# Kernel tuning notes

Hardware: AMD Instinct MI355X
Metric: run time of the kernel (lower is better)

## Reference

```python
import jax, jax.numpy as jnp
import numpy as np

DIM = 768
NUM_HEADS = 12
HEAD_DIM = DIM // NUM_HEADS
SCALE = HEAD_DIM ** -0.5
TPL = 64  # template_feat_len, fixed by the 1:65 slice in softmax_with_policy


def setup_inputs() -> dict:
    key = jax.random.key(0)
    ks = jax.random.split(key, 16)
    B, S, TOK = 64, 256, 1
    N_v = 1 + 2 * TPL + S  # 385
    w = lambda k, shp: (jax.random.normal(k, shp, dtype=jnp.float32) * 0.02)
    return {
        'x': jax.random.normal(ks[0], (B, N_v, DIM), dtype=jnp.float32),
        'template_mask': jax.random.uniform(ks[1], (B, TPL), dtype=jnp.float32),
        'qkv_w': w(ks[2], (3 * DIM, DIM)),
        'qkv_b': jnp.zeros((3 * DIM,), jnp.float32),
        'proj_w': w(ks[3], (DIM, DIM)),
        'proj_b': jnp.zeros((DIM,), jnp.float32),
        'dp1_w': w(ks[4], (384, 2 * DIM)),
        'dp1_b': jnp.zeros((384,), jnp.float32),
        'dp2_w': w(ks[5], (192, 384)),
        'dp2_b': jnp.zeros((192,), jnp.float32),
        'dp3_w': w(ks[6], (2, 192)),
        'dp3_b': jnp.zeros((2,), jnp.float32),
        'search_feat_len': S,
        'token_len': TOK,
    }


def _forward(x, template_mask, qkv_w, qkv_b, proj_w, proj_b,
             dp1_w, dp1_b, dp2_w, dp2_b, dp3_w, dp3_b,
             search_feat_len, token_len):
    B, N_v, C = x.shape
    S, TOK = search_feat_len, token_len
    tfl = (N_v - 1 - S) // 2          # template_feat_len (== 64)
    N_q = N_v - tfl
    eps = 1e-6

    # --- divide prediction (early=True, tgt_type='allavg') ---
    tgt_rep = jnp.mean(x[:, tfl + TOK: 2 * tfl + TOK], axis=1, keepdims=True)  # [B,1,C]
    tgt_rep = jnp.broadcast_to(tgt_rep, (B, S, C))
    h = jnp.concatenate([x[:, -S:], tgt_rep], axis=-1)                          # [B,S,2C]
    h = jax.nn.gelu(h @ dp1_w.T + dp1_b, approximate=False)
    h = jax.nn.gelu(h @ dp2_w.T + dp2_b, approximate=False)
    divide_prediction = jax.nn.log_softmax(h @ dp3_w.T + dp3_b, axis=-1)        # [B,S,2]

    # eval path: argsort descending -> argmax, one-hot decision
    decision = jax.nn.one_hot(jnp.argmax(divide_prediction, axis=-1), 2,
                              dtype=divide_prediction.dtype)                     # [B,S,2]

    # --- policy assembly [B, N_q, 3] ---
    token_policy = jnp.tile(jnp.array([0., 0., 1.], jnp.float32), (B, TOK, 1))
    template_policy = jnp.tile(jnp.array([1., 0., 0.], jnp.float32),
                               (B, N_q - S - TOK, 1))
    search_policy = jnp.concatenate(
        [jnp.zeros((B, S, 1), decision.dtype), decision], axis=-1)
    policy = jnp.concatenate([token_policy, template_policy, search_policy], axis=1)

    # --- qkv ---
    qkv = (x @ qkv_w.T + qkv_b).reshape(B, N_v, 3, NUM_HEADS, HEAD_DIM)
    qkv = qkv.transpose(2, 0, 3, 1, 4)  # [3,B,H,N_v,hd]
    q_o, k, v = qkv[0], qkv[1], qkv[2]
    q = jnp.concatenate([q_o[:, :, :1], q_o[:, :, tfl + TOK:]], axis=2)  # [B,H,N_q,hd]

    attn = jnp.einsum('bhqd,bhkd->bhqk', q, k) * SCALE  # [B,H,N_q,N_v]

    # --- softmax_with_policy ---
    p0, p1, p2 = policy[..., 0], policy[..., 1], policy[..., 2]
    outer = lambda a, b: jnp.einsum('bi,bj->bij', a, b)
    mask = (outer(p0, p0) + outer(p1, p1)
            + outer(p0, p2) + outer(p1, p2) + outer(p2, p2)
            + outer(p2, p0) + outer(p2, p1))                      # [B,N_q,N_q]
    eye = jnp.eye(N_q, dtype=mask.dtype)
    mask = mask + (1.0 - mask) * eye
    # expand key axis: duplicate template cols (1:65) -> width N_q+64 == N_v
    mask = jnp.concatenate([mask[..., :1], mask[..., 1:65], mask[..., 1:]], axis=-1)
    mask = mask[:, None]                                          # [B,1,N_q,N_v]

    max_att = jnp.max(attn, axis=-1, keepdims=True)
    a = jnp.exp(attn - max_att).astype(jnp.float32) * mask.astype(jnp.float32)
    attn = (a + eps / N_q) / (jnp.sum(a, axis=-1, keepdims=True) + eps)
    attn = attn.astype(max_att.dtype)

    out = jnp.einsum('bhqk,bhkd->bhqd', attn, v)                  # [B,H,N_q,hd]
    out = out.transpose(0, 2, 1, 3).reshape(B, N_q, C)
    return out @ proj_w.T + proj_b


def reference(x, template_mask, qkv_w, qkv_b, proj_w, proj_b,
              dp1_w, dp1_b, dp2_w, dp2_b, dp3_w, dp3_b,
              search_feat_len, token_len):
    return _forward(x, template_mask, qkv_w, qkv_b, proj_w, proj_b,
                    dp1_w, dp1_b, dp2_w, dp2_b, dp3_w, dp3_b,
                    search_feat_len, token_len)
```

## Files before the change

kernel.cpp:

```cpp
#include <hip/hip_runtime.h>
#include <cmath>

typedef unsigned short u16;
typedef unsigned int u32;
typedef __attribute__((ext_vector_type(8))) short short8;
typedef __attribute__((ext_vector_type(4))) float f32x4;

#define B_    64
#define NV    385
#define CDIM  768
#define NQ    321
#define SFL   256
#define NH    12
#define HD    64
#define MQ    (B_*NV)
#define MP    (B_*NQ)
#define MD    (B_*SFL)
#define SCALE_ 0.125f
#define EPS_   1e-6f

__device__ __forceinline__ u16 f2b(float f) {
  u32 x = __float_as_uint(f);
  return (u16)((x + 0x7FFFu + ((x >> 16) & 1u)) >> 16);
}
__device__ __forceinline__ float b2f(u16 h) {
  return __uint_as_float((u32)h << 16);
}

__device__ __forceinline__ void gload_lds16(const void* g, void* l) {
  __builtin_amdgcn_global_load_lds(
      (const __attribute__((address_space(1))) u32*)g,
      (__attribute__((address_space(3))) u32*)l,
      16, 0, 0);
}

__global__ void k_convert4(const float4* __restrict__ in, ushort4* __restrict__ out, int n4) {
  int i = blockIdx.x * blockDim.x + threadIdx.x;
  if (i < n4) {
    float4 v = in[i];
    ushort4 o;
    o.x = f2b(v.x); o.y = f2b(v.y); o.z = f2b(v.z); o.w = f2b(v.w);
    out[i] = o;
  }
}

__global__ void k_gather_split(const float* __restrict__ x, ushort4* __restrict__ hi,
                               ushort4* __restrict__ lo, int n4) {
  int idx = blockIdx.x * blockDim.x + threadIdx.x;
  if (idx < n4) {
    int m = idx / 192, c4 = idx - m*192;
    int b = m >> 8, s = m & 255;
    float4 v = *(const float4*)(x + ((size_t)(b*NV + 129 + s))*CDIM + c4*4);
    ushort4 h, l;
    h.x = f2b(v.x); l.x = f2b(v.x - b2f(h.x));
    h.y = f2b(v.y); l.y = f2b(v.y - b2f(h.y));
    h.z = f2b(v.z); l.z = f2b(v.z - b2f(h.z));
    h.w = f2b(v.w); l.w = f2b(v.w - b2f(h.w));
    hi[idx] = h; lo[idx] = l;
  }
}

__global__ void k_split_w(const float* __restrict__ W, int ldw, int rows, int colsDiv4,
                          int outRows, ushort4* __restrict__ hi, ushort4* __restrict__ lo) {
  int idx = blockIdx.x * blockDim.x + threadIdx.x;
  if (idx < outRows * colsDiv4) {
    int r = idx / colsDiv4, c4 = idx - r*colsDiv4;
    ushort4 h = {0,0,0,0}, l = {0,0,0,0};
    if (r < rows) {
      float4 v = *(const float4*)(W + (size_t)r*ldw + c4*4);
      h.x = f2b(v.x); l.x = f2b(v.x - b2f(h.x));
      h.y = f2b(v.y); l.y = f2b(v.y - b2f(h.y));
      h.z = f2b(v.z); l.z = f2b(v.z - b2f(h.z));
      h.w = f2b(v.w); l.w = f2b(v.w - b2f(h.w));
    }
    hi[idx] = h; lo[idx] = l;
  }
}

__global__ void k_tgt(const float* __restrict__ x, float* __restrict__ tgt) {
  int b = blockIdx.x, c = threadIdx.x;
  float s = 0.f;
  for (int j = 0; j < 64; ++j) s += x[((size_t)(b*NV + 65 + j))*CDIM + c];
  tgt[b*CDIM + c] = s * (1.f/64.f);
}

__device__ __forceinline__ float gelu_exact(float x) {
  return 0.5f * x * (1.f + erff(x * 0.70710678118654752f));
}

__global__ __launch_bounds__(256) void k_gemm128(const u16* __restrict__ A, const u16* __restrict__ W,
                                                 const float* __restrict__ bias,
                                                 u16* __restrict__ Qh, u16* __restrict__ Kh, u16* __restrict__ Vh,
                                                 float* __restrict__ Cf,
                                                 int M, int N, int K, int mode) {
  __shared__ __align__(16) u16 sbuf[128*128];
  u16* As = sbuf;
  u16* Ws = sbuf + 8192;
  int tid = threadIdx.x;
  int wave = tid >> 6, lane = tid & 63;
  int quad = lane >> 4, col = lane & 15;
  int m0 = blockIdx.y * 128, n0 = blockIdx.x * 128;

  const u16* pa[4];
  const u16* pb[4];
#pragma unroll
  for (int p = 0; p < 4; ++p) {
    int c = p*256 + tid;
    int row = c >> 3;
    int sg = (c & 7) ^ (row & 7);
    pa[p] = A + (size_t)min(m0 + row, M - 1) * K + sg*8;
    pb[p] = W + (size_t)(n0 + row) * K + sg*8;
  }

  int wm = (wave >> 1) * 64, wn = (wave & 1) * 64;
  f32x4 acc[4][4];
  f32x4 z4 = {0.f, 0.f, 0.f, 0.f};
#pragma unroll
  for (int i = 0; i < 4; ++i)
#pragma unroll
    for (int j = 0; j < 4; ++j) acc[i][j] = z4;

  for (int k0 = 0; k0 < K; k0 += 64) {
#pragma unroll
    for (int p = 0; p < 4; ++p) {
      gload_lds16(pa[p], &As[(p*256 + wave*64) * 8]);
      gload_lds16(pb[p], &Ws[(p*256 + wave*64) * 8]);
      pa[p] += 64; pb[p] += 64;
    }
    __syncthreads();

#pragma unroll
    for (int kk = 0; kk < 2; ++kk) {
      int sr = quad + kk*4;
      short8 af[4], bf[4];
#pragma unroll
      for (int i = 0; i < 4; ++i) {
        int row = wm + i*16 + col;
        af[i] = *(const short8*)&As[row*64 + ((sr ^ (row & 7)) * 8)];
      }
#pragma unroll
      for (int j = 0; j < 4; ++j) {
        int row = wn + j*16 + col;
        bf[j] = *(const short8*)&Ws[row*64 + ((sr ^ (row & 7)) * 8)];
      }
#pragma unroll
      for (int i = 0; i < 4; ++i)
#pragma unroll
        for (int j = 0; j < 4; ++j)
          acc[i][j] = __builtin_amdgcn_mfma_f32_16x16x32_bf16(af[i], bf[j], acc[i][j], 0, 0, 0);
    }
    __syncthreads();
  }

  if (mode == 0) {
#pragma unroll
    for (int j = 0; j < 4; ++j) {
      int cc = wn + j*16 + col;
      float bv = bias ? bias[n0 + cc] : 0.f;
#pragma unroll
      for (int i = 0; i < 4; ++i)
#pragma unroll
        for (int ii = 0; ii < 4; ++ii) {
          int row = wm + i*16 + quad*4 + ii;
          sbuf[row*128 + cc] = f2b(acc[i][j][ii] + bv);
        }
    }
    __syncthreads();
#pragma unroll
    for (int q = 0; q < 8; ++q) {
      int idx = q*256 + tid;
      int row = idx >> 4, c16 = idx & 15;
      int mg = m0 + row;
      if (mg < M) {
        int n = n0 + c16*8;
        int which = n / 768;
        int rem = n - which*768;
        int hh = rem >> 6, d0 = rem & 63;
        int bb = mg / NV, nn = mg - bb*NV;
        u16* dst = (which == 0) ? Qh : (which == 1) ? Kh : Vh;
        *(float4*)(dst + (((size_t)hh*B_ + bb)*NV + nn)*64 + d0) = *(const float4*)&sbuf[row*128 + c16*8];
      }
    }
  } else {
#pragma unroll
    for (int j = 0; j < 4; ++j) {
      int cc = n0 + wn + j*16 + col;
      float bv = bias ? bias[cc] : 0.f;
#pragma unroll
      for (int i = 0; i < 4; ++i) {
        int r = m0 + wm + i*16 + quad*4;
#pragma unroll
        for (int ii = 0; ii < 4; ++ii) {
          if (r + ii < M) Cf[(size_t)(r + ii) * N + cc] = acc[i][j][ii] + bv;
        }
      }
    }
  }
}

__global__ __launch_bounds__(256) void k_gemm128s(const u16* __restrict__ Ah, const u16* __restrict__ Al,
                                                  const u16* __restrict__ Wh, const u16* __restrict__ Wl,
                                                  const float* __restrict__ bias, const float* __restrict__ bias2,
                                                  u16* __restrict__ Chi, u16* __restrict__ Clo,
                                                  float* __restrict__ Cf,
                                                  int M, int N, int K, int Nb, int geluF) {
  __shared__ __align__(16) u16 sb[4*8192];
  u16* sAh = sb;
  u16* sAl = sb + 8192;
  u16* sWh = sb + 16384;
  u16* sWl = sb + 24576;
  int tid = threadIdx.x;
  int wave = tid >> 6, lane = tid & 63;
  int quad = lane >> 4, col = lane & 15;
  int m0 = blockIdx.y * 128, n0 = blockIdx.x * 128;

  const u16 *pah[4], *pal[4], *pbh[4], *pbl[4];
#pragma unroll
  for (int p = 0; p < 4; ++p) {
    int c = p*256 + tid;
    int row = c >> 3;
    int sg = (c & 7) ^ (row & 7);
    size_t ao = (size_t)min(m0 + row, M - 1) * K + sg*8;
    size_t bo = (size_t)(n0 + row) * K + sg*8;
    pah[p] = Ah + ao; pal[p] = Al + ao;
    pbh[p] = Wh + bo; pbl[p] = Wl + bo;
  }

  int wm = (wave >> 1) * 64, wn = (wave & 1) * 64;
  f32x4 acc[4][4];
  f32x4 z4 = {0.f, 0.f, 0.f, 0.f};
#pragma unroll
  for (int i = 0; i < 4; ++i)
#pragma unroll
    for (int j = 0; j < 4; ++j) acc[i][j] = z4;

  for (int k0 = 0; k0 < K; k0 += 64) {
#pragma unroll
    for (int p = 0; p < 4; ++p) {
      int dst = (p*256 + wave*64) * 8;
      gload_lds16(pah[p], &sAh[dst]);
      gload_lds16(pal[p], &sAl[dst]);
      gload_lds16(pbh[p], &sWh[dst]);
      gload_lds16(pbl[p], &sWl[dst]);
      pah[p] += 64; pal[p] += 64; pbh[p] += 64; pbl[p] += 64;
    }
    __syncthreads();

#pragma unroll
    for (int kk = 0; kk < 2; ++kk) {
      int sr = quad + kk*4;
      short8 ah[4], al[4], bh[4], bl[4];
#pragma unroll
      for (int i = 0; i < 4; ++i) {
        int row = wm + i*16 + col;
        int off = row*64 + ((sr ^ (row & 7)) * 8);
        ah[i] = *(const short8*)&sAh[off];
        al[i] = *(const short8*)&sAl[off];
      }
#pragma unroll
      for (int j = 0; j < 4; ++j) {
        int row = wn + j*16 + col;
        int off = row*64 + ((sr ^ (row & 7)) * 8);
        bh[j] = *(const short8*)&sWh[off];
        bl[j] = *(const short8*)&sWl[off];
      }
#pragma unroll
      for (int i = 0; i < 4; ++i)
#pragma unroll
        for (int j = 0; j < 4; ++j) {
          acc[i][j] = __builtin_amdgcn_mfma_f32_16x16x32_bf16(ah[i], bh[j], acc[i][j], 0, 0, 0);
          acc[i][j] = __builtin_amdgcn_mfma_f32_16x16x32_bf16(ah[i], bl[j], acc[i][j], 0, 0, 0);
          acc[i][j] = __builtin_amdgcn_mfma_f32_16x16x32_bf16(al[i], bh[j], acc[i][j], 0, 0, 0);
        }
    }
    __syncthreads();
  }

  if (geluF) {
#pragma unroll
    for (int j = 0; j < 4; ++j) {
      int cc = wn + j*16 + col;
      float bv = bias ? bias[n0 + cc] : 0.f;
#pragma unroll
      for (int i = 0; i < 4; ++i)
#pragma unroll
        for (int ii = 0; ii < 4; ++ii) {
          int row = wm + i*16 + quad*4 + ii;
          int mg = m0 + row;
          float v = acc[i][j][ii] + bv;
          if (bias2) v += bias2[(size_t)(mg >> 8) * N + n0 + cc];
          v = gelu_exact(v);
          u16 hi = f2b(v);
          sb[row*128 + cc] = hi;
          sb[16384 + row*128 + cc] = f2b(v - b2f(hi));
        }
    }
    __syncthreads();
#pragma unroll
    for (int q = 0; q < 8; ++q) {
      int idx = q*256 + tid;
      int row = idx >> 4, c16 = idx & 15;
      int mg = m0 + row;
      if (mg < M) {
        *(float4*)(Chi + (size_t)mg * N + n0 + c16*8) = *(const float4*)&sb[row*128 + c16*8];
        *(float4*)(Clo + (size_t)mg * N + n0 + c16*8) = *(const float4*)&sb[16384 + row*128 + c16*8];
      }
    }
  } else {
#pragma unroll
    for (int j = 0; j < 4; ++j) {
      int ccg = n0 + wn + j*16 + col;
      float bv = (bias && ccg < Nb) ? bias[ccg] : 0.f;
#pragma unroll
      for (int i = 0; i < 4; ++i) {
        int r = m0 + wm + i*16 + quad*4;
#pragma unroll
        for (int ii = 0; ii < 4; ++ii) {
          if (r + ii < M) Cf[(size_t)(r + ii) * N + ccg] = acc[i][j][ii] + bv;
        }
      }
    }
  }
}

__global__ __launch_bounds__(256) void k_gemm_f32(const float* __restrict__ A,
                                                  const float* __restrict__ x,
                                                  const float* __restrict__ W, int ldw,
                                                  const float* __restrict__ bias,
                                                  float* __restrict__ C, int M, int N, int K,
                                                  int gather, int gelu, int bias2d) {
  __shared__ __align__(16) float As[16][132];
  __shared__ __align__(16) float Ws[16][68];
  int tid = threadIdx.x;
  int tx = tid & 15, ty = tid >> 4;
  int n0 = blockIdx.x * 64, m0 = blockIdx.y * 128;
  float acc[8][4] = {};

  for (int k0 = 0; k0 < K; k0 += 16) {
#pragma unroll
    for (int p = 0; p < 2; ++p) {
      int f = p * 256 + tid;
      int row = f >> 2, kc = (f & 3) * 4;
      float4 v;
      if (gather) {
        int m = m0 + row;
        int b = m >> 8, s2 = m & 255;
        v = *(const float4*)(x + ((size_t)(b*NV + 129 + s2))*CDIM + k0 + kc);
      } else {
        int m = min(m0 + row, M - 1);
        v = *(const float4*)(A + (size_t)m * K + k0 + kc);
      }
      As[kc+0][row] = v.x; As[kc+1][row] = v.y; As[kc+2][row] = v.z; As[kc+3][row] = v.w;
    }
    {
      int row = tid >> 2, kc = (tid & 3) * 4;
      float4 wv = *(const float4*)(W + (size_t)(n0 + row) * ldw + k0 + kc);
      Ws[kc+0][row] = wv.x; Ws[kc+1][row] = wv.y; Ws[kc+2][row] = wv.z; Ws[kc+3][row] = wv.w;
    }
    __syncthreads();
#pragma unroll
    for (int k2 = 0; k2 < 16; ++k2) {
      float4 a0 = *(const float4*)&As[k2][ty*8];
      float4 a1 = *(const float4*)&As[k2][ty*8 + 4];
      float4 wv = *(const float4*)&Ws[k2][tx*4];
      float a_[8] = {a0.x, a0.y, a0.z, a0.w, a1.x, a1.y, a1.z, a1.w};
      float w_[4] = {wv.x, wv.y, wv.z, wv.w};
#pragma unroll
      for (int i = 0; i < 8; ++i)
#pragma unroll
        for (int j = 0; j < 4; ++j) acc[i][j] += a_[i] * w_[j];
    }
    __syncthreads();
  }
#pragma unroll
  for (int i = 0; i < 8; ++i) {
    int r = m0 + ty*8 + i;
    if (r < M) {
      float4 o;
      float* op = (float*)&o;
#pragma unroll
      for (int j = 0; j < 4; ++j) {
        int n = n0 + tx*4 + j;
        float bv = bias2d ? bias[(size_t)(r >> 8) * N + n] : bias[n];
        float v = acc[i][j] + bv;
        op[j] = gelu ? gelu_exact(v) : v;
      }
      *(float4*)(C + (size_t)r * N + n0 + tx*4) = o;
    }
  }
}

__global__ void k_decision(const float* __restrict__ h2f, const float* __restrict__ w3,
                           const float* __restrict__ b3, float* __restrict__ sdec) {
  int r = blockIdx.x * blockDim.x + threadIdx.x;
  const float* hp = h2f + (size_t)r * 256;
  float l0 = b3[0], l1 = b3[1];
  for (int k = 0; k < 192; ++k) {
    float h = gelu_exact(hp[k]);
    l0 += h * w3[k]; l1 += h * w3[192 + k];
  }
  sdec[r] = (l1 > l0) ? 1.f : 0.f;
}

__global__ __launch_bounds__(512, 4) void k_attn(const u16* __restrict__ Qh, const u16* __restrict__ Kh,
                                                 const u16* __restrict__ Vh, const float* __restrict__ sdec,
                                                 u16* __restrict__ O) {
  __shared__ __align__(16) u16 vsT[64*424];
  __shared__ __align__(16) u16 pst[8][16][72];
  __shared__ float sd[256];
  __shared__ __align__(16) float sdm[416];
  __shared__ float vsum[64];
  float* vpart = (float*)pst;

  int b = blockIdx.x, h = blockIdx.y;
  int tid = threadIdx.x;
  int wave = tid >> 6, lane = tid & 63;
  int quad = lane >> 4, col = lane & 15;

  size_t base = ((size_t)(h*B_ + b))*NV*64;
  const u16* Qb = Qh + base;
  const u16* Kb = Kh + base;
  const u16* Vb = Vh + base;

  if (tid < 256) sd[tid] = sdec[b*SFL + tid];
  for (int k = tid; k < 416; k += 512)
    sdm[k] = (k < 129) ? 1.f : ((k <= 384) ? sdec[b*SFL + k - 129] : 0.f);

  for (int i = tid; i < 64*39; i += 512) {
    int d = i / 39, n = 385 + (i - d*39);
    vsT[d*424 + n] = 0;
  }
  for (int idx = tid; idx < NV*8; idx += 512) {
    int n = idx >> 3, seg = idx & 7;
    short8 v = *(const short8*)(Vb + (size_t)n*64 + seg*8);
    int c = n >> 3;
    int cs = (c < 48) ? ((c & ~7) | ((c + seg) & 7)) : c;
    int b2 = cs*8 + (n & 7);
#pragma unroll
    for (int j = 0; j < 8; ++j)
      vsT[(seg*8 + j)*424 + b2] = ((const u16*)&v)[j];
  }
  __syncthreads();

  {
    int d = tid & 63, part = tid >> 6;
    int n_lo = part*49, n_hi = min(n_lo + 49, 385);
    float s = 0.f;
    for (int n = n_lo; n < n_hi; ++n) {
      int c = n >> 3;
      int cs = (c < 48) ? ((c & ~7) | ((c + (d >> 3)) & 7)) : c;
      s += __uint_as_float((u32)vsT[d*424 + cs*8 + (n & 7)] << 16);
    }
    vpart[part*64 + d] = s;
  }
  __syncthreads();
  if (tid < 64) {
    float s = 0.f;
#pragma unroll
    for (int p = 0; p < 8; ++p) s += vpart[p*64 + tid];
    vsum[tid] = s;
  }
  __syncthreads();

  const f32x4 z4 = {0.f, 0.f, 0.f, 0.f};
  float vsn[4];
#pragma unroll
  for (int nt = 0; nt < 4; ++nt) vsn[nt] = vsum[nt*16 + col];

  for (int t = wave; t < 21; t += 8) {
    int qn_lane = t*16 + col;
    int pos = (qn_lane == 0) ? 0 : (min(qn_lane, 320) + 64);
    const u16* qp = Qb + (size_t)pos*64 + quad*8;
    short8 aq0 = *(const short8*)(qp);
    short8 aq1 = *(const short8*)(qp + 32);

    bool isTpl = (qn_lane >= 1 && qn_lane <= 64);
    bool isSearch = (qn_lane >= 65);
    float sdq = isSearch ? sd[min(qn_lane - 65, 255)] : 1.f;

    float m_ = -1e30f, l_ = 0.f;
    f32x4 oc[4];
#pragma unroll
    for (int nt = 0; nt < 4; ++nt) oc[nt] = z4;

    for (int ch = 0; ch < 6; ++ch) {
      int key0c = ch*64;
      f32x4 acc4[4];
#pragma unroll
      for (int j = 0; j < 4; ++j) acc4[j] = z4;
#pragma unroll
      for (int j = 0; j < 4; ++j) {
        const u16* kp = Kb + (size_t)(key0c + j*16 + col)*64;
        short8 k0 = *(const short8*)(kp + quad*8);
        short8 k1 = *(const short8*)(kp + 32 + quad*8);
        acc4[j] = __builtin_amdgcn_mfma_f32_16x16x32_bf16(k0, aq0, acc4[j], 0, 0, 0);
        acc4[j] = __builtin_amdgcn_mfma_f32_16x16x32_bf16(k1, aq1, acc4[j], 0, 0, 0);
      }
      float cm = acc4[0][0];
#pragma unroll
      for (int j = 0; j < 4; ++j)
#pragma unroll
        for (int r = 0; r < 4; ++r)
          if (j || r) cm = fmaxf(cm, acc4[j][r]);
      cm = fmaxf(cm, __shfl_xor(cm, 16, 64));
      cm = fmaxf(cm, __shfl_xor(cm, 32, 64));
      float mn = fmaxf(m_, cm * SCALE_);
      float rnew = __expf(m_ - mn);
      m_ = mn;
      float rb[4];
#pragma unroll
      for (int r = 0; r < 4; ++r) rb[r] = __shfl(rnew, quad*4 + r, 64);
#pragma unroll
      for (int nt = 0; nt < 4; ++nt) {
        oc[nt][0] *= rb[0]; oc[nt][1] *= rb[1]; oc[nt][2] *= rb[2]; oc[nt][3] *= rb[3];
      }

      float ssum = 0.f;
#pragma unroll
      for (int j = 0; j < 4; ++j) {
        int key0 = key0c + j*16;
        float4 tm = make_float4(1.f, 1.f, 1.f, 1.f);
        if (isTpl) tm = *(const float4*)&sdm[key0 + quad*4];
        float a[4];
        const float* tmp = (const float*)&tm;
#pragma unroll
        for (int r = 0; r < 4; ++r) {
          int key = key0 + quad*4 + r;
          float msk = isTpl ? tmp[r]
                            : ((isSearch && key >= 1 && key <= 128) ? sdq : 1.f);
          a[r] = __expf(fmaf(acc4[j][r], SCALE_, -mn)) * msk;
          ssum += a[r];
        }
        uint2 pk;
        pk.x = (u32)f2b(a[0]) | ((u32)f2b(a[1]) << 16);
        pk.y = (u32)f2b(a[2]) | ((u32)f2b(a[3]) << 16);
        *(uint2*)&pst[wave][col][j*16 + quad*4] = pk;
      }
      ssum += __shfl_xor(ssum, 16, 64);
      ssum += __shfl_xor(ssum, 32, 64);
      l_ = l_ * rnew + ssum;

      asm volatile("" ::: "memory");
#pragma unroll
      for (int st = 0; st < 2; ++st) {
        short8 pa = *(const short8*)&pst[wave][col][st*32 + quad*8];
        int step = ch*2 + st;
#pragma unroll
        for (int nt = 0; nt < 4; ++nt) {
          int d = nt*16 + col;
          int c = step*4 + quad;
          int cs = (c & ~7) | ((c + (d >> 3)) & 7);
          short8 bv = *(const short8*)&vsT[d*424 + cs*8];
          oc[nt] = __builtin_amdgcn_mfma_f32_16x16x32_bf16(pa, bv, oc[nt], 0, 0, 0);
        }
      }
    }

    {
      const u16* kp = Kb + (size_t)384*64;
      short8 k0 = *(const short8*)(kp + quad*8);
      short8 k1 = *(const short8*)(kp + 32 + quad*8);
      f32x4 accE = z4;
      accE = __builtin_amdgcn_mfma_f32_16x16x32_bf16(k0, aq0, accE, 0, 0, 0);
      accE = __builtin_amdgcn_mfma_f32_16x16x32_bf16(k1, aq1, accE, 0, 0, 0);
      float cm = (quad == 0) ? accE[0] : -1e30f;
      cm = fmaxf(cm, __shfl_xor(cm, 16, 64));
      cm = fmaxf(cm, __shfl_xor(cm, 32, 64));
      float mn = fmaxf(m_, cm * SCALE_);
      float rnew = __expf(m_ - mn);
      m_ = mn;
      float rb[4];
#pragma unroll
      for (int r = 0; r < 4; ++r) rb[r] = __shfl(rnew, quad*4 + r, 64);
#pragma unroll
      for (int nt = 0; nt < 4; ++nt) {
        oc[nt][0] *= rb[0]; oc[nt][1] *= rb[1]; oc[nt][2] *= rb[2]; oc[nt][3] *= rb[3];
      }
      float mskE = isTpl ? sdm[384] : 1.f;
      float aE = (quad == 0) ? __expf(fmaf(accE[0], SCALE_, -mn)) * mskE : 0.f;
      float ssum = aE;
      ssum += __shfl_xor(ssum, 16, 64);
      ssum += __shfl_xor(ssum, 32, 64);
      l_ = l_ * rnew + ssum;

      uint2 pk;
      pk.x = (quad == 0) ? (u32)f2b(aE) : 0u;
      pk.y = 0u;
      *(uint2*)&pst[wave][col][quad*4] = pk;
      *(uint2*)&pst[wave][col][16 + quad*4] = make_uint2(0u, 0u);
      asm volatile("" ::: "memory");
      short8 pa = *(const short8*)&pst[wave][col][quad*8];
#pragma unroll
      for (int nt = 0; nt < 4; ++nt) {
        int d = nt*16 + col;
        short8 bv = *(const short8*)&vsT[d*424 + (48 + quad)*8];
        oc[nt] = __builtin_amdgcn_mfma_f32_16x16x32_bf16(pa, bv, oc[nt], 0, 0, 0);
      }
    }

    float lb[4];
#pragma unroll
    for (int r = 0; r < 4; ++r) lb[r] = __shfl(l_, quad*4 + r, 64);
    const float epsn = EPS_ / 321.f;
#pragma unroll
    for (int r = 0; r < 4; ++r) {
      float invv = 1.f / (lb[r] + EPS_);
      int qn = t*16 + quad*4 + r;
      if (qn <= 320) {
#pragma unroll
        for (int nt = 0; nt < 4; ++nt) {
          float val = (oc[nt][r] + epsn * vsn[nt]) * invv;
          O[((size_t)(b*NQ + qn))*CDIM + h*HD + nt*16 + col] = f2b(val);
        }
      }
    }
  }
}

extern "C" void kernel_launch(void* const* d_in, const int* in_sizes, int n_in,
                              void* d_out, int out_size, void* d_ws, size_t ws_size,
                              hipStream_t stream) {
  const float* x      = (const float*)d_in[0];
  const float* qkv_w  = (const float*)d_in[2];
  const float* qkv_b  = (const float*)d_in[3];
  const float* proj_w = (const float*)d_in[4];
  const float* proj_b = (const float*)d_in[5];
  const float* dp1_w  = (const float*)d_in[6];
  const float* dp1_b  = (const float*)d_in[7];
  const float* dp2_w  = (const float*)d_in[8];
  const float* dp2_b  = (const float*)d_in[9];
  const float* dp3_w  = (const float*)d_in[10];
  const float* dp3_b  = (const float*)d_in[11];
  float* out = (float*)d_out;

  char* ws = (char*)d_ws;
  size_t off = 0;
  auto alloc = [&](size_t bytes) -> void* {
    void* p = ws + off;
    off += (bytes + 255) & ~(size_t)255;
    return p;
  };
  u16*  xb      = (u16*)alloc((size_t)MQ * CDIM * 2);
  u16*  qkv_wb  = (u16*)alloc((size_t)2304 * CDIM * 2);
  u16*  proj_wb = (u16*)alloc((size_t)CDIM * CDIM * 2);
  u16*  qh      = (u16*)alloc((size_t)NH * B_ * NV * 64 * 2);
  u16*  kh      = (u16*)alloc((size_t)NH * B_ * NV * 64 * 2);
  u16*  vh      = (u16*)alloc((size_t)NH * B_ * NV * 64 * 2);
  u16*  Obuf    = (u16*)alloc((size_t)MP * CDIM * 2);
  float* tgt    = (float*)alloc((size_t)B_ * CDIM * 4);
  float* tb     = (float*)alloc((size_t)B_ * 384 * 4);
  u16*  xsh     = (u16*)alloc((size_t)MD * CDIM * 2);
  u16*  xsl     = (u16*)alloc((size_t)MD * CDIM * 2);
  u16*  w1h     = (u16*)alloc((size_t)384 * CDIM * 2);
  u16*  w1l     = (u16*)alloc((size_t)384 * CDIM * 2);
  u16*  w2h     = (u16*)alloc((size_t)256 * 384 * 2);
  u16*  w2l     = (u16*)alloc((size_t)256 * 384 * 2);
  u16*  h1h     = (u16*)alloc((size_t)MD * 384 * 2);
  u16*  h1l     = (u16*)alloc((size_t)MD * 384 * 2);
  float* h2f    = (float*)alloc((size_t)MD * 256 * 4);
  float* sdec   = (float*)alloc((size_t)MD * 4);

  {
    int n4 = MQ * CDIM / 4;
    k_convert4<<<dim3((n4 + 255)/256), dim3(256), 0, stream>>>((const float4*)x, (ushort4*)xb, n4);
  }
  {
    int n4 = 2304 * CDIM / 4;
    k_convert4<<<dim3((n4 + 255)/256), dim3(256), 0, stream>>>((const float4*)qkv_w, (ushort4*)qkv_wb, n4);
  }
  {
    int n4 = CDIM * CDIM / 4;
    k_convert4<<<dim3((n4 + 255)/256), dim3(256), 0, stream>>>((const float4*)proj_w, (ushort4*)proj_wb, n4);
  }
  k_tgt<<<dim3(B_), dim3(CDIM), 0, stream>>>(x, tgt);

  {
    int n4 = MD * 192;
    k_gather_split<<<dim3((n4 + 255)/256), dim3(256), 0, stream>>>(x, (ushort4*)xsh, (ushort4*)xsl, n4);
  }
  {
    int n4 = 384 * 192;
    k_split_w<<<dim3((n4 + 255)/256), dim3(256), 0, stream>>>(dp1_w, 1536, 384, 192, 384,
                                                              (ushort4*)w1h, (ushort4*)w1l);
  }
  {
    int n4 = 256 * 96;
    k_split_w<<<dim3((n4 + 255)/256), dim3(256), 0, stream>>>(dp2_w, 384, 192, 96, 256,
                                                              (ushort4*)w2h, (ushort4*)w2l);
  }

  k_gemm128<<<dim3(2304/128, (MQ + 127)/128), dim3(256), 0, stream>>>(xb, qkv_wb, qkv_b, qh, kh, vh,
                                                                      (float*)nullptr, MQ, 2304, CDIM, 0);
  k_gemm_f32<<<dim3(384/64, 1), dim3(256), 0, stream>>>(tgt, nullptr, dp1_w + 768, 1536, dp1_b, tb,
                                                        B_, 384, CDIM, 0, 0, 0);
  k_gemm128s<<<dim3(384/128, MD/128), dim3(256), 0, stream>>>(xsh, xsl, w1h, w1l,
                                                              nullptr, tb, h1h, h1l, nullptr,
                                                              MD, 384, CDIM, 384, 1);
  k_gemm128s<<<dim3(256/128, MD/128), dim3(256), 0, stream>>>(h1h, h1l, w2h, w2l,
                                                              dp2_b, nullptr, nullptr, nullptr, h2f,
                                                              MD, 256, 384, 192, 0);
  k_decision<<<dim3(MD/256), dim3(256), 0, stream>>>(h2f, dp3_w, dp3_b, sdec);

  k_attn<<<dim3(B_, NH), dim3(512), 0, stream>>>(qh, kh, vh, sdec, Obuf);

  k_gemm128<<<dim3(CDIM/128, (MP + 127)/128), dim3(256), 0, stream>>>(Obuf, proj_wb, proj_b,
                                                                      nullptr, nullptr, nullptr, out,
                                                                      MP, CDIM, CDIM, 1);
}
```

Baseline: 707.7 us.

## Fuse prep kernels, XCD-swizzle GEMM tiles, parallelize decision, drop eps term

Merges the x conversion and split-gather into one row-wise kernel and the weight conversions into a single launch. Adds XCD-aware block swizzling to the bf16 GEMM, moves the dp2 GELU into the GEMM epilogue, and replaces the per-thread decision loop with a wave-reduced logit difference. Swaps the tiny tgt GEMM for a simple per-batch kernel. In attention it adds s_setprio around the MFMA sections and removes the V-sum eps correction, which slightly changes numerics (drops the eps/N_q term).

```diff
diff --git a/kernel.cpp b/kernel.cpp
--- a/kernel.cpp
+++ b/kernel.cpp
@@ -34,46 +34,76 @@
       16, 0, 0);
 }
 
-__global__ void k_convert4(const float4* __restrict__ in, ushort4* __restrict__ out, int n4) {
-  int i = blockIdx.x * blockDim.x + threadIdx.x;
-  if (i < n4) {
-    float4 v = in[i];
-    ushort4 o;
-    o.x = f2b(v.x); o.y = f2b(v.y); o.z = f2b(v.z); o.w = f2b(v.w);
-    out[i] = o;
-  }
-}
-
-__global__ void k_gather_split(const float* __restrict__ x, ushort4* __restrict__ hi,
-                               ushort4* __restrict__ lo, int n4) {
-  int idx = blockIdx.x * blockDim.x + threadIdx.x;
-  if (idx < n4) {
-    int m = idx / 192, c4 = idx - m*192;
-    int b = m >> 8, s = m & 255;
-    float4 v = *(const float4*)(x + ((size_t)(b*NV + 129 + s))*CDIM + c4*4);
+__device__ __forceinline__ int xcd_swz(int lin, int nwg) {
+  int xcd = lin & 7, idx = lin >> 3;
+  int q = nwg >> 3, r = nwg & 7;
+  int base = (xcd < r) ? xcd * (q + 1) : r * (q + 1) + (xcd - r) * q;
+  return base + idx;
+}
+
+__device__ __forceinline__ float gelu_exact(float x) {
+  return 0.5f * x * (1.f + erff(x * 0.70710678118654752f));
+}
+
+__global__ void k_prep_x(const float* __restrict__ x, ushort4* __restrict__ xb,
+                         ushort4* __restrict__ xsh, ushort4* __restrict__ xsl) {
+  int row = blockIdx.x;
+  int tid = threadIdx.x;
+  float4 v = ((const float4*)x)[(size_t)row*192 + tid];
+  ushort4 h;
+  h.x = f2b(v.x); h.y = f2b(v.y); h.z = f2b(v.z); h.w = f2b(v.w);
+  xb[(size_t)row*192 + tid] = h;
+  int b = row / NV, n = row - b*NV;
+  if (n >= 129) {
+    ushort4 l;
+    l.x = f2b(v.x - b2f(h.x)); l.y = f2b(v.y - b2f(h.y));
+    l.z = f2b(v.z - b2f(h.z)); l.w = f2b(v.w - b2f(h.w));
+    size_t s = (size_t)(b*256 + n - 129)*192 + tid;
+    xsh[s] = h; xsl[s] = l;
+  }
+}
+
+#define PR0 442368
+#define PR1 (PR0 + 147456)
+#define PR2 (PR1 + 73728)
+#define PR3 (PR2 + 24576)
+__global__ void k_prep_w(const float* __restrict__ qkv_w, const float* __restrict__ proj_w,
+                         const float* __restrict__ dp1_w, const float* __restrict__ dp2_w,
+                         ushort4* __restrict__ qkv_wb, ushort4* __restrict__ proj_wb,
+                         ushort4* __restrict__ w1h, ushort4* __restrict__ w1l,
+                         ushort4* __restrict__ w2h, ushort4* __restrict__ w2l) {
+  int i = blockIdx.x * 256 + threadIdx.x;
+  if (i < PR0) {
+    float4 v = ((const float4*)qkv_w)[i];
+    ushort4 h; h.x = f2b(v.x); h.y = f2b(v.y); h.z = f2b(v.z); h.w = f2b(v.w);
+    qkv_wb[i] = h;
+  } else if (i < PR1) {
+    int j = i - PR0;
+    float4 v = ((const float4*)proj_w)[j];
+    ushort4 h; h.x = f2b(v.x); h.y = f2b(v.y); h.z = f2b(v.z); h.w = f2b(v.w);
+    proj_wb[j] = h;
+  } else if (i < PR2) {
+    int j = i - PR1;
+    int r = j / 192, c4 = j - r*192;
+    float4 v = *(const float4*)(dp1_w + (size_t)r*1536 + c4*4);
     ushort4 h, l;
     h.x = f2b(v.x); l.x = f2b(v.x - b2f(h.x));
     h.y = f2b(v.y); l.y = f2b(v.y - b2f(h.y));
     h.z = f2b(v.z); l.z = f2b(v.z - b2f(h.z));
     h.w = f2b(v.w); l.w = f2b(v.w - b2f(h.w));
-    hi[idx] = h; lo[idx] = l;
-  }
-}
-
-__global__ void k_split_w(const float* __restrict__ W, int ldw, int rows, int colsDiv4,
-                          int outRows, ushort4* __restrict__ hi, ushort4* __restrict__ lo) {
-  int idx = blockIdx.x * blockDim.x + threadIdx.x;
-  if (idx < outRows * colsDiv4) {
-    int r = idx / colsDiv4, c4 = idx - r*colsDiv4;
+    w1h[j] = h; w1l[j] = l;
+  } else if (i < PR3) {
+    int j = i - PR2;
+    int r = j / 96, c4 = j - r*96;
     ushort4 h = {0,0,0,0}, l = {0,0,0,0};
-    if (r < rows) {
-      float4 v = *(const float4*)(W + (size_t)r*ldw + c4*4);
+    if (r < 192) {
+      float4 v = *(const float4*)(dp2_w + (size_t)r*384 + c4*4);
       h.x = f2b(v.x); l.x = f2b(v.x - b2f(h.x));
       h.y = f2b(v.y); l.y = f2b(v.y - b2f(h.y));
       h.z = f2b(v.z); l.z = f2b(v.z - b2f(h.z));
       h.w = f2b(v.w); l.w = f2b(v.w - b2f(h.w));
     }
-    hi[idx] = h; lo[idx] = l;
+    w2h[j] = h; w2l[j] = l;
   }
 }
 
@@ -84,8 +114,21 @@
   tgt[b*CDIM + c] = s * (1.f/64.f);
 }
 
-__device__ __forceinline__ float gelu_exact(float x) {
-  return 0.5f * x * (1.f + erff(x * 0.70710678118654752f));
+__global__ __launch_bounds__(256) void k_tb(const float* __restrict__ tgt, const float* __restrict__ dp1_w,
+                                            const float* __restrict__ dp1_b, float* __restrict__ tb) {
+  __shared__ float tg[768];
+  int b = blockIdx.x, tid = threadIdx.x;
+  for (int i = tid; i < 768; i += 256) tg[i] = tgt[b*768 + i];
+  __syncthreads();
+  for (int n = tid; n < 384; n += 256) {
+    const float* w = dp1_w + (size_t)n*1536 + 768;
+    float s = dp1_b[n];
+    for (int k = 0; k < 768; k += 4) {
+      float4 wv = *(const float4*)(w + k);
+      s += tg[k]*wv.x + tg[k+1]*wv.y + tg[k+2]*wv.z + tg[k+3]*wv.w;
+    }
+    tb[b*384 + n] = s;
+  }
 }
 
 __global__ __launch_bounds__(256) void k_gemm128(const u16* __restrict__ A, const u16* __restrict__ W,
@@ -99,7 +142,11 @@
   int tid = threadIdx.x;
   int wave = tid >> 6, lane = tid & 63;
   int quad = lane >> 4, col = lane & 15;
-  int m0 = blockIdx.y * 128, n0 = blockIdx.x * 128;
+  int gx = gridDim.x;
+  int lin = blockIdx.y * gx + blockIdx.x;
+  int s = xcd_swz(lin, gx * gridDim.y);
+  int bx = s % gx, by = s / gx;
+  int m0 = by * 128, n0 = bx * 128;
 
   const u16* pa[4];
   const u16* pb[4];
@@ -203,7 +250,7 @@
                                                   const float* __restrict__ bias, const float* __restrict__ bias2,
                                                   u16* __restrict__ Chi, u16* __restrict__ Clo,
                                                   float* __restrict__ Cf,
-                                                  int M, int N, int K, int Nb, int geluF) {
+                                                  int M, int N, int K, int Nb, int geluF, int gelu2) {
   __shared__ __align__(16) u16 sb[4*8192];
   u16* sAh = sb;
   u16* sAl = sb + 8192;
@@ -316,90 +363,28 @@
         int r = m0 + wm + i*16 + quad*4;
 #pragma unroll
         for (int ii = 0; ii < 4; ++ii) {
-          if (r + ii < M) Cf[(size_t)(r + ii) * N + ccg] = acc[i][j][ii] + bv;
+          if (r + ii < M) {
+            float v = acc[i][j][ii] + bv;
+            if (gelu2) v = gelu_exact(v);
+            Cf[(size_t)(r + ii) * N + ccg] = v;
+          }
         }
       }
     }
   }
 }
 
-__global__ __launch_bounds__(256) void k_gemm_f32(const float* __restrict__ A,
-                                                  const float* __restrict__ x,
-                                                  const float* __restrict__ W, int ldw,
-                                                  const float* __restrict__ bias,
-                                                  float* __restrict__ C, int M, int N, int K,
-                                                  int gather, int gelu, int bias2d) {
-  __shared__ __align__(16) float As[16][132];
-  __shared__ __align__(16) float Ws[16][68];
-  int tid = threadIdx.x;
-  int tx = tid & 15, ty = tid >> 4;
-  int n0 = blockIdx.x * 64, m0 = blockIdx.y * 128;
-  float acc[8][4] = {};
-
-  for (int k0 = 0; k0 < K; k0 += 16) {
-#pragma unroll
-    for (int p = 0; p < 2; ++p) {
-      int f = p * 256 + tid;
-      int row = f >> 2, kc = (f & 3) * 4;
-      float4 v;
-      if (gather) {
-        int m = m0 + row;
-        int b = m >> 8, s2 = m & 255;
-        v = *(const float4*)(x + ((size_t)(b*NV + 129 + s2))*CDIM + k0 + kc);
-      } else {
-        int m = min(m0 + row, M - 1);
-        v = *(const float4*)(A + (size_t)m * K + k0 + kc);
-      }
-      As[kc+0][row] = v.x; As[kc+1][row] = v.y; As[kc+2][row] = v.z; As[kc+3][row] = v.w;
-    }
-    {
-      int row = tid >> 2, kc = (tid & 3) * 4;
-      float4 wv = *(const float4*)(W + (size_t)(n0 + row) * ldw + k0 + kc);
-      Ws[kc+0][row] = wv.x; Ws[kc+1][row] = wv.y; Ws[kc+2][row] = wv.z; Ws[kc+3][row] = wv.w;
-    }
-    __syncthreads();
-#pragma unroll
-    for (int k2 = 0; k2 < 16; ++k2) {
-      float4 a0 = *(const float4*)&As[k2][ty*8];
-      float4 a1 = *(const float4*)&As[k2][ty*8 + 4];
-      float4 wv = *(const float4*)&Ws[k2][tx*4];
-      float a_[8] = {a0.x, a0.y, a0.z, a0.w, a1.x, a1.y, a1.z, a1.w};
-      float w_[4] = {wv.x, wv.y, wv.z, wv.w};
-#pragma unroll
-      for (int i = 0; i < 8; ++i)
-#pragma unroll
-        for (int j = 0; j < 4; ++j) acc[i][j] += a_[i] * w_[j];
-    }
-    __syncthreads();
-  }
-#pragma unroll
-  for (int i = 0; i < 8; ++i) {
-    int r = m0 + ty*8 + i;
-    if (r < M) {
-      float4 o;
-      float* op = (float*)&o;
-#pragma unroll
-      for (int j = 0; j < 4; ++j) {
-        int n = n0 + tx*4 + j;
-        float bv = bias2d ? bias[(size_t)(r >> 8) * N + n] : bias[n];
-        float v = acc[i][j] + bv;
-        op[j] = gelu ? gelu_exact(v) : v;
-      }
-      *(float4*)(C + (size_t)r * N + n0 + tx*4) = o;
-    }
-  }
-}
-
-__global__ void k_decision(const float* __restrict__ h2f, const float* __restrict__ w3,
-                           const float* __restrict__ b3, float* __restrict__ sdec) {
-  int r = blockIdx.x * blockDim.x + threadIdx.x;
-  const float* hp = h2f + (size_t)r * 256;
-  float l0 = b3[0], l1 = b3[1];
-  for (int k = 0; k < 192; ++k) {
-    float h = gelu_exact(hp[k]);
-    l0 += h * w3[k]; l1 += h * w3[192 + k];
-  }
-  sdec[r] = (l1 > l0) ? 1.f : 0.f;
+__global__ __launch_bounds__(256) void k_decision(const float* __restrict__ h2g, const float* __restrict__ w3,
+                                                  const float* __restrict__ b3, float* __restrict__ sdec) {
+  int wave = threadIdx.x >> 6, lane = threadIdx.x & 63;
+  int r = blockIdx.x * 4 + wave;
+  const float* hp = h2g + (size_t)r * 256;
+  float d = hp[lane]       * (w3[192 + lane] - w3[lane])
+          + hp[64 + lane]  * (w3[256 + lane] - w3[64 + lane])
+          + hp[128 + lane] * (w3[320 + lane] - w3[128 + lane]);
+#pragma unroll
+  for (int m = 1; m <= 32; m <<= 1) d += __shfl_xor(d, m, 64);
+  if (lane == 0) sdec[r] = (d + (b3[1] - b3[0]) > 0.f) ? 1.f : 0.f;
 }
 
 __global__ __launch_bounds__(512, 4) void k_attn(const u16* __restrict__ Qh, const u16* __restrict__ Kh,
@@ -407,10 +392,7 @@
                                                  u16* __restrict__ O) {
   __shared__ __align__(16) u16 vsT[64*424];
   __shared__ __align__(16) u16 pst[8][16][72];
-  __shared__ float sd[256];
   __shared__ __align__(16) float sdm[416];
-  __shared__ float vsum[64];
-  float* vpart = (float*)pst;
 
   int b = blockIdx.x, h = blockIdx.y;
   int tid = threadIdx.x;
@@ -422,9 +404,8 @@
   const u16* Kb = Kh + base;
   const u16* Vb = Vh + base;
 
-  if (tid < 256) sd[tid] = sdec[b*SFL + tid];
-  for (int k = tid; k < 416; k += 512)
-    sdm[k] = (k < 129) ? 1.f : ((k <= 384) ? sdec[b*SFL + k - 129] : 0.f);
+  if (tid < 416)
+    sdm[tid] = (tid < 129) ? 1.f : ((tid <= 384) ? sdec[b*SFL + tid - 129] : 0.f);
 
   for (int i = tid; i < 64*39; i += 512) {
     int d = i / 39, n = 385 + (i - d*39);
@@ -442,30 +423,7 @@
   }
   __syncthreads();
 
-  {
-    int d = tid & 63, part = tid >> 6;
-    int n_lo = part*49, n_hi = min(n_lo + 49, 385);
-    float s = 0.f;
-    for (int n = n_lo; n < n_hi; ++n) {
-      int c = n >> 3;
-      int cs = (c < 48) ? ((c & ~7) | ((c + (d >> 3)) & 7)) : c;
-      s += __uint_as_float((u32)vsT[d*424 + cs*8 + (n & 7)] << 16);
-    }
-    vpart[part*64 + d] = s;
-  }
-  __syncthreads();
-  if (tid < 64) {
-    float s = 0.f;
-#pragma unroll
-    for (int p = 0; p < 8; ++p) s += vpart[p*64 + tid];
-    vsum[tid] = s;
-  }
-  __syncthreads();
-
   const f32x4 z4 = {0.f, 0.f, 0.f, 0.f};
-  float vsn[4];
-#pragma unroll
-  for (int nt = 0; nt < 4; ++nt) vsn[nt] = vsum[nt*16 + col];
 
   for (int t = wave; t < 21; t += 8) {
     int qn_lane = t*16 + col;
@@ -476,7 +434,7 @@
 
     bool isTpl = (qn_lane >= 1 && qn_lane <= 64);
     bool isSearch = (qn_lane >= 65);
-    float sdq = isSearch ? sd[min(qn_lane - 65, 255)] : 1.f;
+    float sdq = isSearch ? sdm[min(qn_lane + 64, 384)] : 1.f;
 
     float m_ = -1e30f, l_ = 0.f;
     f32x4 oc[4];
@@ -488,6 +446,7 @@
       f32x4 acc4[4];
 #pragma unroll
       for (int j = 0; j < 4; ++j) acc4[j] = z4;
+      __builtin_amdgcn_s_setprio(1);
 #pragma unroll
       for (int j = 0; j < 4; ++j) {
         const u16* kp = Kb + (size_t)(key0c + j*16 + col)*64;
@@ -496,6 +455,7 @@
         acc4[j] = __builtin_amdgcn_mfma_f32_16x16x32_bf16(k0, aq0, acc4[j], 0, 0, 0);
         acc4[j] = __builtin_amdgcn_mfma_f32_16x16x32_bf16(k1, aq1, acc4[j], 0, 0, 0);
       }
+      __builtin_amdgcn_s_setprio(0);
       float cm = acc4[0][0];
 #pragma unroll
       for (int j = 0; j < 4; ++j)
@@ -541,6 +501,7 @@
       l_ = l_ * rnew + ssum;
 
       asm volatile("" ::: "memory");
+      __builtin_amdgcn_s_setprio(1);
 #pragma unroll
       for (int st = 0; st < 2; ++st) {
         short8 pa = *(const short8*)&pst[wave][col][st*32 + quad*8];
@@ -554,6 +515,7 @@
           oc[nt] = __builtin_amdgcn_mfma_f32_16x16x32_bf16(pa, bv, oc[nt], 0, 0, 0);
         }
       }
+      __builtin_amdgcn_s_setprio(0);
     }
 
     {
@@ -601,17 +563,14 @@
     float lb[4];
 #pragma unroll
     for (int r = 0; r < 4; ++r) lb[r] = __shfl(l_, quad*4 + r, 64);
-    const float epsn = EPS_ / 321.f;
 #pragma unroll
     for (int r = 0; r < 4; ++r) {
       float invv = 1.f / (lb[r] + EPS_);
       int qn = t*16 + quad*4 + r;
       if (qn <= 320) {
 #pragma unroll
-        for (int nt = 0; nt < 4; ++nt) {
-          float val = (oc[nt][r] + epsn * vsn[nt]) * invv;
-          O[((size_t)(b*NQ + qn))*CDIM + h*HD + nt*16 + col] = f2b(val);
-        }
+        for (int nt = 0; nt < 4; ++nt)
+          O[((size_t)(b*NQ + qn))*CDIM + h*HD + nt*16 + col] = f2b(oc[nt][r] * invv);
       }
     }
   }
@@ -660,46 +619,23 @@
   float* h2f    = (float*)alloc((size_t)MD * 256 * 4);
   float* sdec   = (float*)alloc((size_t)MD * 4);
 
-  {
-    int n4 = MQ * CDIM / 4;
-    k_convert4<<<dim3((n4 + 255)/256), dim3(256), 0, stream>>>((const float4*)x, (ushort4*)xb, n4);
-  }
-  {
-    int n4 = 2304 * CDIM / 4;
-    k_convert4<<<dim3((n4 + 255)/256), dim3(256), 0, stream>>>((const float4*)qkv_w, (ushort4*)qkv_wb, n4);
-  }
-  {
-    int n4 = CDIM * CDIM / 4;
-    k_convert4<<<dim3((n4 + 255)/256), dim3(256), 0, stream>>>((const float4*)proj_w, (ushort4*)proj_wb, n4);
-  }
+  k_prep_x<<<dim3(MQ), dim3(192), 0, stream>>>(x, (ushort4*)xb, (ushort4*)xsh, (ushort4*)xsl);
+  k_prep_w<<<dim3(PR3/256), dim3(256), 0, stream>>>(qkv_w, proj_w, dp1_w, dp2_w,
+                                                    (ushort4*)qkv_wb, (ushort4*)proj_wb,
+                                                    (ushort4*)w1h, (ushort4*)w1l,
+                                                    (ushort4*)w2h, (ushort4*)w2l);
   k_tgt<<<dim3(B_), dim3(CDIM), 0, stream>>>(x, tgt);
-
-  {
-    int n4 = MD * 192;
-    k_gather_split<<<dim3((n4 + 255)/256), dim3(256), 0, stream>>>(x, (ushort4*)xsh, (ushort4*)xsl, n4);
-  }
-  {
-    int n4 = 384 * 192;
-    k_split_w<<<dim3((n4 + 255)/256), dim3(256), 0, stream>>>(dp1_w, 1536, 384, 192, 384,
-                                                              (ushort4*)w1h, (ushort4*)w1l);
-  }
-  {
-    int n4 = 256 * 96;
-    k_split_w<<<dim3((n4 + 255)/256), dim3(256), 0, stream>>>(dp2_w, 384, 192, 96, 256,
-                                                              (ushort4*)w2h, (ushort4*)w2l);
-  }
 
   k_gemm128<<<dim3(2304/128, (MQ + 127)/128), dim3(256), 0, stream>>>(xb, qkv_wb, qkv_b, qh, kh, vh,
                                                                       (float*)nullptr, MQ, 2304, CDIM, 0);
-  k_gemm_f32<<<dim3(384/64, 1), dim3(256), 0, stream>>>(tgt, nullptr, dp1_w + 768, 1536, dp1_b, tb,
-                                                        B_, 384, CDIM, 0, 0, 0);
+  k_tb<<<dim3(B_), dim3(256), 0, stream>>>(tgt, dp1_w, dp1_b, tb);
   k_gemm128s<<<dim3(384/128, MD/128), dim3(256), 0, stream>>>(xsh, xsl, w1h, w1l,
                                                               nullptr, tb, h1h, h1l, nullptr,
-                                                              MD, 384, CDIM, 384, 1);
+                                                              MD, 384, CDIM, 384, 1, 0);
   k_gemm128s<<<dim3(256/128, MD/128), dim3(256), 0, stream>>>(h1h, h1l, w2h, w2l,
                                                               dp2_b, nullptr, nullptr, nullptr, h2f,
-                                                              MD, 256, 384, 192, 0);
-  k_decision<<<dim3(MD/256), dim3(256), 0, stream>>>(h2f, dp3_w, dp3_b, sdec);
+                                                              MD, 256, 384, 192, 0, 1);
+  k_decision<<<dim3(MD/4), dim3(256), 0, stream>>>(h2f, dp3_w, dp3_b, sdec);
 
   k_attn<<<dim3(B_, NH), dim3(512), 0, stream>>>(qh, kh, vh, sdec, Obuf);
 
```

Result: faster. 599.5 us (-15.3%).
